# Kernel optimization log

Measured on AMD Instinct MI355X. Metric: run time of the kernel, lower is better.

The kernel has to match this reference:

```python
import jax, jax.numpy as jnp
import numpy as np

N_WIRES = 10
N_BLOCKS = 4
DIM = 2 ** N_WIRES


def _tables(n):
    # Basis-state bit tables. Wire 0 is the most-significant bit (torchquantum convention).
    s = np.arange(2 ** n)
    bits = (s[None, :] >> (n - 1 - np.arange(n))[:, None]) & 1  # [n, 2^n]
    zval = (1 - 2 * bits).astype(np.float32)  # PauliZ eigenvalue per wire per basis state
    # Composition of the circular CNOT ring (0,1),(1,2),...,(n-2,n-1),(n-1,0)
    # as a single basis permutation: state'[s] = state[P[s]].
    pairs = [(i, i + 1) for i in range(n - 1)] + [(n - 1, 0)]
    P = s.copy()
    for c, t in pairs:
        bit = (s >> (n - 1 - c)) & 1
        g = s ^ (bit << (n - 1 - t))  # CNOT maps new[s] = old[g(s)]
        P = P[g]
    return zval, P


_ZVAL_NP, _PERM_NP = _tables(N_WIRES)


def setup_inputs() -> dict:
    key = jax.random.key(0)
    k1, k2 = jax.random.split(key)
    x = jax.random.normal(k1, (2048, N_WIRES), jnp.float32)
    params = jax.random.normal(k2, (N_BLOCKS, 6, N_WIRES), jnp.float32)
    return {"x": x, "params": params}


def _rz_all(state, theta, zval):
    # RZ(theta_w) on every wire fused into one diagonal phase over the full statevector.
    # RZ = diag(e^{-i t/2}, e^{+i t/2}); exponent sign = -zval (bit0 -> -1).
    phase = jnp.exp((-0.5j) * (theta @ zval).astype(jnp.complex64))  # [2^n]
    return state * phase[None, :]


def _ry_all(state, theta, bsz):
    # RY(theta_w) on each wire w: 2x2 rotation applied along that wire's axis.
    for w in range(N_WIRES):
        left = 2 ** w
        right = DIM // (2 * left)
        s4 = state.reshape(bsz, left, 2, right)
        c = jnp.cos(theta[w] * 0.5)
        s_ = jnp.sin(theta[w] * 0.5)
        U = jnp.stack([jnp.stack([c, -s_]), jnp.stack([s_, c])]).astype(jnp.complex64)
        s4 = jnp.einsum('bixk,jx->bijk', s4, U)
        state = s4.reshape(bsz, DIM)
    return state


def reference(x, params):
    zval = jnp.asarray(_ZVAL_NP)
    perm = jnp.asarray(_PERM_NP)
    bsz = x.shape[0]
    state = jnp.zeros((bsz, DIM), jnp.complex64).at[:, 0].set(1.0)  # |0...0>
    for k in range(N_BLOCKS):
        p = params[k]
        # NOTE: the original module's "rx" layers are constructed with tq.RZ,
        # so each block is RZ, RY, RZ, CNOT-ring, RZ, RY, RZ, CNOT-ring.
        state = _rz_all(state, p[0], zval)
        state = _ry_all(state, p[1], bsz)
        state = _rz_all(state, p[2], zval)
        state = state[:, perm]
        state = _rz_all(state, p[3], zval)
        state = _ry_all(state, p[4], bsz)
        state = _rz_all(state, p[5], zval)
        state = state[:, perm]
        if k != N_BLOCKS - 1:
            # data re-uploading encoder: RZ(x[:, w]) on wire w, batch-dependent diagonal
            enc = jnp.exp((-0.5j) * (x @ zval).astype(jnp.complex64))  # [B, 2^n]
            state = state * enc
    probs = state.real ** 2 + state.imag ** 2  # [B, 2^n]
    out = probs @ zval.T  # MeasureAll PauliZ -> [B, n_wires]
    return out[None]  # [1, B, n_wires]
```

## Files before the change

### kernel.cpp

```cpp
#include <hip/hip_runtime.h>

#define NW 10

typedef float v2f __attribute__((ext_vector_type(2)));
typedef float v4f __attribute__((ext_vector_type(4)));

template<int CTRL>
__device__ __forceinline__ float fdpp(float v) {
    return __int_as_float(__builtin_amdgcn_mov_dpp(__float_as_int(v), CTRL, 0xF, 0xF, true));
}
template<int PAT>
__device__ __forceinline__ float fswz(float v) {
    return __int_as_float(__builtin_amdgcn_ds_swizzle(__float_as_int(v), PAT));
}

__device__ __forceinline__ int sC(int W, int lane, int r) { return (W << 8) | (lane << 2) | r; }
__device__ __forceinline__ int sL1(int W, int lane, int r) {
    return ((r & 1) << 8) | (((r >> 1) & 1) << 9)
         | ((lane & 1) << 4) | (((lane >> 1) & 1) << 6) | (((lane >> 2) & 1) << 2)
         | (((lane >> 3) & 1) << 7) | (((lane >> 4) & 1) << 3) | (((lane >> 5) & 1) << 5)
         | ((W & 1) << 0) | (((W >> 1) & 1) << 1);
}
__device__ __forceinline__ int phi(int e) {
    return e ^ ((e & 0x10) >> 1) ^ ((e & 0x20) >> 4);
}

__global__ void precompute_kernel(const float* __restrict__ params, float4* __restrict__ tab4) {
    const int d = blockIdx.x;
    const int j = threadIdx.x;
    if (d < 14) {
        int k, row; bool L1;
        if (d < 3)       { k = d + 1;  row = 0; L1 = false; }
        else if (d < 7)  { k = d - 3;  row = 2; L1 = true;  }
        else if (d < 11) { k = d - 7;  row = 3; L1 = false; }
        else             { k = d - 11; row = 5; L1 = true;  }
        const float* th = params + (k * 6 + row) * NW;
        const int W = j >> 8, lane = j & 63, r = (j >> 6) & 3;
        const int s = L1 ? sL1(W, lane, r) : sC(W, lane, r);
        float ang = 0.f;
#pragma unroll
        for (int w = 0; w < NW; ++w)
            ang += th[w] * (((s >> (9 - w)) & 1) ? 0.5f : -0.5f);
        float sn, cs;
        __sincosf(ang, &sn, &cs);
        tab4[d * 1024 + j] = make_float4(cs, sn, -sn, cs);
    } else if (j < 80) {
        const int ry = j / NW, w = j % NW;
        const int k = ry >> 1, i = ry & 1;
        const float* th = params + (k * 6 + (i ? 4 : 1)) * NW;
        float sn, cs;
        __sincosf(0.5f * th[w], &sn, &cs);
        float2* ryt = (float2*)(tab4 + 14 * 1024);
        ryt[j] = make_float2(cs, sn);
    }
}

__global__ __launch_bounds__(256, 4) void qsim_kernel(const float* __restrict__ x,
                                                      const v4f* __restrict__ tab4,
                                                      float* __restrict__ out) {
    __shared__ v2f buf[2][1024];
    __shared__ float sred[4][NW];

    const int t     = threadIdx.x;
    const int W     = t >> 6;
    const int lane  = t & 63;
    const int b     = blockIdx.x;
    const int ebase = lane | (W << 8);
    const float2* ry_tab = (const float2*)(tab4 + 14 * 1024);

    v2f st[4];
#pragma unroll
    for (int r = 0; r < 4; ++r) st[r] = (v2f){0.f, 0.f};
    if (t == 0) st[0].x = 1.f;

    const int wbase = phi(ebase);
    const int l0 = lane & 1, l1 = (lane >> 1) & 1, l2 = (lane >> 2) & 1,
              l3 = (lane >> 3) & 1, l4 = (lane >> 4) & 1, l5 = (lane >> 5) & 1;
    const int W0 = W & 1, W1 = (W >> 1) & 1;
    const int riA0 = l2 | (l4 << 1) | (l0 << 2) | (l5 << 3) | (l1 << 4) | (l3 << 5) | (W << 6);
    const int rgA  = phi(riA0);
    const int g0 = (l2 ^ l3) | ((l4 ^ l5) << 1) | ((l0 ^ l1) << 2) | ((l5 ^ W0) << 3)
                 | ((l1 ^ l2) << 4) | ((l3 ^ l4) << 5)
                 | ((W0 ^ W1) << 6) | (W1 << 7) | (l0 << 9);
    const int gP = phi(g0);

    const float* xb = x + b * NW;
    v2f xp[4];
    {
        float xv[NW];
#pragma unroll
        for (int w = 0; w < NW; ++w) xv[w] = xb[w];
        float A = 0.f;
#pragma unroll
        for (int w = 0; w < NW; ++w) A += xv[w];
        float hi = -0.5f * A;
        if (W & 2) hi += xv[0];
        if (W & 1) hi += xv[1];
#pragma unroll
        for (int j = 0; j < 6; ++j)
            hi += ((lane >> j) & 1) ? xv[7 - j] : 0.f;
        float lo[4];
        lo[0] = 0.f;   lo[1] = xv[9];
        lo[2] = xv[8]; lo[3] = xv[8] + xv[9];
#pragma unroll
        for (int r = 0; r < 4; ++r) {
            float sn, cs;
            __sincosf(hi + lo[r], &sn, &cs);
            xp[r] = (v2f){cs, sn};
        }
    }

    int bs = 0;
    v4f tq[4];

    auto pre = [&](int d) {
        const v4f* tb = tab4 + (d << 10) + ebase;
#pragma unroll
        for (int r = 0; r < 4; ++r) tq[r] = tb[r << 6];
    };
    auto apply_t = [&]() {
#pragma unroll
        for (int r = 0; r < 4; ++r)
            st[r] = st[r].x * tq[r].xy + st[r].y * tq[r].zw;
    };
    auto apply_tx = [&]() {
#pragma unroll
        for (int r = 0; r < 4; ++r) {
            const v2f c = xp[r].x * tq[r].xy + xp[r].y * tq[r].zw;
            const v2f cq = (v2f){-c.y, c.x};
            st[r] = st[r].x * c + st[r].y * cq;
        }
    };

    auto bfly_local = [&](float2 cw, int m) {
#pragma unroll
        for (int r = 0; r < 4; ++r) {
            if (!(r & m)) {
                const int r2 = r | m;
                const v2f a = st[r];
                st[r]  = cw.x * a - cw.y * st[r2];
                st[r2] = cw.y * a + cw.x * st[r2];
            }
        }
    };

    auto ry = [&](int ridx) {
        const float2* rt = ry_tab + ridx * NW;
        bfly_local(rt[9], 1);
        bfly_local(rt[8], 2);
        {   const float2 cw = rt[7]; const float ss = (lane & 1) ? cw.y : -cw.y;
#pragma unroll
            for (int r = 0; r < 4; ++r) {
                v2f p; p.x = fdpp<0xB1>(st[r].x); p.y = fdpp<0xB1>(st[r].y);
                st[r] = cw.x * st[r] + ss * p;
            }
        }
        {   const float2 cw = rt[6]; const float ss = (lane & 2) ? cw.y : -cw.y;
#pragma unroll
            for (int r = 0; r < 4; ++r) {
                v2f p; p.x = fdpp<0x4E>(st[r].x); p.y = fdpp<0x4E>(st[r].y);
                st[r] = cw.x * st[r] + ss * p;
            }
        }
        {   const float2 cw = rt[4]; const float ss = (lane & 8) ? cw.y : -cw.y;
#pragma unroll
            for (int r = 0; r < 4; ++r) {
                v2f p; p.x = fdpp<0x128>(st[r].x); p.y = fdpp<0x128>(st[r].y);
                st[r] = cw.x * st[r] + ss * p;
            }
        }
        {
            v2f* B = buf[bs]; bs ^= 1;
#pragma unroll
            for (int r = 0; r < 4; ++r)
                B[wbase + (r << 6)] = st[r];
            __syncthreads();
#pragma unroll
            for (int r = 0; r < 4; ++r)
                st[r] = B[rgA + (r << 8)];
        }
        bfly_local(rt[1], 1);
        bfly_local(rt[0], 2);
        {   const float2 cw = rt[5]; const float ss = (lane & 1) ? cw.y : -cw.y;
#pragma unroll
            for (int r = 0; r < 4; ++r) {
                v2f p; p.x = fdpp<0xB1>(st[r].x); p.y = fdpp<0xB1>(st[r].y);
                st[r] = cw.x * st[r] + ss * p;
            }
        }
        {   const float2 cw = rt[3]; const float ss = (lane & 2) ? cw.y : -cw.y;
#pragma unroll
            for (int r = 0; r < 4; ++r) {
                v2f p; p.x = fdpp<0x4E>(st[r].x); p.y = fdpp<0x4E>(st[r].y);
                st[r] = cw.x * st[r] + ss * p;
            }
        }
        {   const float2 cw = rt[2]; const float ss = (lane & 8) ? cw.y : -cw.y;
#pragma unroll
            for (int r = 0; r < 4; ++r) {
                v2f p; p.x = fdpp<0x128>(st[r].x); p.y = fdpp<0x128>(st[r].y);
                st[r] = cw.x * st[r] + ss * p;
            }
        }
    };

    auto perm = [&]() {
        v2f* B = buf[bs]; bs ^= 1;
#pragma unroll
        for (int r = 0; r < 4; ++r)
            B[wbase + (r << 6)] = st[r];
        __syncthreads();
        constexpr int xc[4] = {0, 0x1C0, 0x300, 0x2C0};
#pragma unroll
        for (int r = 0; r < 4; ++r)
            st[r] = B[gP ^ xc[r]];
    };

#pragma unroll 1
    for (int k = 0; k < 4; ++k) {
        if (k > 0) apply_tx();
        pre(3 + k);
        ry(2 * k);
        apply_t();
        pre(7 + k);
        perm();
        apply_t();
        if (k < 3) pre(11 + k);
        ry(2 * k + 1);
        if (k < 3) { apply_t(); pre(k); }
        perm();
    }

    float pr[4];
#pragma unroll
    for (int r = 0; r < 4; ++r) pr[r] = st[r].x * st[r].x + st[r].y * st[r].y;
    float S = 0.f;
#pragma unroll
    for (int r = 0; r < 4; ++r) S += pr[r];

    float acc[NW];
    acc[0] = (W & 2) ? -S : S;
    acc[1] = (W & 1) ? -S : S;
#pragma unroll
    for (int w = 2; w <= 7; ++w) {
        const int j = 7 - w;
        acc[w] = ((lane >> j) & 1) ? -S : S;
    }
    {
        float t8 = 0.f, t9 = 0.f;
#pragma unroll
        for (int r = 0; r < 4; ++r) {
            t8 += (r & 2) ? -pr[r] : pr[r];
            t9 += (r & 1) ? -pr[r] : pr[r];
        }
        acc[8] = t8; acc[9] = t9;
    }
#pragma unroll
    for (int w = 0; w < NW; ++w) {
        float a = acc[w];
        a += fdpp<0xB1>(a);
        a += fdpp<0x4E>(a);
        a += fswz<0x101F>(a);
        a += fdpp<0x128>(a);
        a += fswz<0x401F>(a);
        a += __shfl_xor(a, 32, 64);
        acc[w] = a;
    }
    if (lane == 0) {
#pragma unroll
        for (int w = 0; w < NW; ++w) sred[W][w] = acc[w];
    }
    __syncthreads();
    if (t < NW) out[b * NW + t] = sred[0][t] + sred[1][t] + sred[2][t] + sred[3][t];
}

extern "C" void kernel_launch(void* const* d_in, const int* in_sizes, int n_in,
                              void* d_out, int out_size, void* d_ws, size_t ws_size,
                              hipStream_t stream) {
    const float* x      = (const float*)d_in[0];
    const float* params = (const float*)d_in[1];
    float* out          = (float*)d_out;
    float4* tab4        = (float4*)d_ws;
    (void)in_sizes; (void)n_in; (void)out_size; (void)ws_size;
    precompute_kernel<<<15, 1024, 0, stream>>>(params, tab4);
    qsim_kernel<<<2048, 256, 0, stream>>>(x, (const v4f*)tab4, out);
}
```

Baseline: 83.49 us.

## Change statevector register layout for vectorized LDS writes and skip final permutation

Thread t now owns four contiguous basis states instead of lane-strided ones. This lets each thread store its registers to LDS as two 16-byte writes with a new XOR swizzle, and lets phase tables load as contiguous float4s. The last CNOT-ring permutation and its barrier are dropped. The permutation is instead folded into the final PauliZ measurement through XOR parity signs. The new index mapping must be exactly consistent across the RY exchange, the permutation and the table generation, or results are wrong.

Measured after the change: 85.77 us. 2.7% more time.

```diff
diff --git a/kernel.cpp b/kernel.cpp
--- a/kernel.cpp
+++ b/kernel.cpp
@@ -14,16 +14,13 @@
     return __int_as_float(__builtin_amdgcn_ds_swizzle(__float_as_int(v), PAT));
 }
 
-__device__ __forceinline__ int sC(int W, int lane, int r) { return (W << 8) | (lane << 2) | r; }
 __device__ __forceinline__ int sL1(int W, int lane, int r) {
     return ((r & 1) << 8) | (((r >> 1) & 1) << 9)
          | ((lane & 1) << 4) | (((lane >> 1) & 1) << 6) | (((lane >> 2) & 1) << 2)
          | (((lane >> 3) & 1) << 7) | (((lane >> 4) & 1) << 3) | (((lane >> 5) & 1) << 5)
          | ((W & 1) << 0) | (((W >> 1) & 1) << 1);
 }
-__device__ __forceinline__ int phi(int e) {
-    return e ^ ((e & 0x10) >> 1) ^ ((e & 0x20) >> 4);
-}
+__device__ __forceinline__ int phiA(int a) { return a ^ ((a & 0x50) >> 3); }
 
 __global__ void precompute_kernel(const float* __restrict__ params, float4* __restrict__ tab4) {
     const int d = blockIdx.x;
@@ -35,8 +32,7 @@
         else if (d < 11) { k = d - 7;  row = 3; L1 = false; }
         else             { k = d - 11; row = 5; L1 = true;  }
         const float* th = params + (k * 6 + row) * NW;
-        const int W = j >> 8, lane = j & 63, r = (j >> 6) & 3;
-        const int s = L1 ? sL1(W, lane, r) : sC(W, lane, r);
+        const int s = L1 ? sL1(j >> 8, (j >> 2) & 63, j & 3) : j;
         float ang = 0.f;
 #pragma unroll
         for (int w = 0; w < NW; ++w)
@@ -58,14 +54,13 @@
 __global__ __launch_bounds__(256, 4) void qsim_kernel(const float* __restrict__ x,
                                                       const v4f* __restrict__ tab4,
                                                       float* __restrict__ out) {
-    __shared__ v2f buf[2][1024];
+    __shared__ __align__(16) v2f buf[2][1024];
     __shared__ float sred[4][NW];
 
     const int t     = threadIdx.x;
     const int W     = t >> 6;
     const int lane  = t & 63;
     const int b     = blockIdx.x;
-    const int ebase = lane | (W << 8);
     const float2* ry_tab = (const float2*)(tab4 + 14 * 1024);
 
     v2f st[4];
@@ -73,16 +68,16 @@
     for (int r = 0; r < 4; ++r) st[r] = (v2f){0.f, 0.f};
     if (t == 0) st[0].x = 1.f;
 
-    const int wbase = phi(ebase);
     const int l0 = lane & 1, l1 = (lane >> 1) & 1, l2 = (lane >> 2) & 1,
               l3 = (lane >> 3) & 1, l4 = (lane >> 4) & 1, l5 = (lane >> 5) & 1;
     const int W0 = W & 1, W1 = (W >> 1) & 1;
-    const int riA0 = l2 | (l4 << 1) | (l0 << 2) | (l5 << 3) | (l1 << 4) | (l3 << 5) | (W << 6);
-    const int rgA  = phi(riA0);
-    const int g0 = (l2 ^ l3) | ((l4 ^ l5) << 1) | ((l0 ^ l1) << 2) | ((l5 ^ W0) << 3)
-                 | ((l1 ^ l2) << 4) | ((l3 ^ l4) << 5)
-                 | ((W0 ^ W1) << 6) | (W1 << 7) | (l0 << 9);
-    const int gP = phi(g0);
+
+    const int wb4 = (t << 1) ^ (l4 << 2) ^ l2;
+    const int rgA2 = phiA(sL1(W, lane, 0));
+    const int abase = (W0 ^ W1) | (W1 << 1) | ((l2 ^ l3) << 2) | ((l4 ^ l5) << 3)
+                    | ((l0 ^ l1) << 4) | ((l5 ^ W0) << 5) | ((l1 ^ l2) << 6)
+                    | ((l3 ^ l4) << 7) | (l0 << 9);
+    const int gP2 = phiA(abase);
 
     const float* xb = x + b * NW;
     v2f xp[4];
@@ -114,9 +109,9 @@
     v4f tq[4];
 
     auto pre = [&](int d) {
-        const v4f* tb = tab4 + (d << 10) + ebase;
-#pragma unroll
-        for (int r = 0; r < 4; ++r) tq[r] = tb[r << 6];
+        const v4f* tb = tab4 + (d << 10) + (t << 2);
+#pragma unroll
+        for (int r = 0; r < 4; ++r) tq[r] = tb[r];
     };
     auto apply_t = [&]() {
 #pragma unroll
@@ -144,6 +139,12 @@
         }
     };
 
+    auto lds_write_own = [&](v2f* B) {
+        v4f* B4 = (v4f*)B;
+        B4[wb4]     = (v4f){st[0].x, st[0].y, st[1].x, st[1].y};
+        B4[wb4 ^ 1] = (v4f){st[2].x, st[2].y, st[3].x, st[3].y};
+    };
+
     auto ry = [&](int ridx) {
         const float2* rt = ry_tab + ridx * NW;
         bfly_local(rt[9], 1);
@@ -171,13 +172,11 @@
         }
         {
             v2f* B = buf[bs]; bs ^= 1;
+            lds_write_own(B);
+            __syncthreads();
 #pragma unroll
             for (int r = 0; r < 4; ++r)
-                B[wbase + (r << 6)] = st[r];
-            __syncthreads();
-#pragma unroll
-            for (int r = 0; r < 4; ++r)
-                st[r] = B[rgA + (r << 8)];
+                st[r] = B[rgA2 + (r << 8)];
         }
         bfly_local(rt[1], 1);
         bfly_local(rt[0], 2);
@@ -206,14 +205,12 @@
 
     auto perm = [&]() {
         v2f* B = buf[bs]; bs ^= 1;
+        lds_write_own(B);
+        __syncthreads();
+        constexpr int xq[4] = {0, 0x103, 0x300, 0x203};
 #pragma unroll
         for (int r = 0; r < 4; ++r)
-            B[wbase + (r << 6)] = st[r];
-        __syncthreads();
-        constexpr int xc[4] = {0, 0x1C0, 0x300, 0x2C0};
-#pragma unroll
-        for (int r = 0; r < 4; ++r)
-            st[r] = B[gP ^ xc[r]];
+            st[r] = B[gP2 ^ xq[r]];
     };
 
 #pragma unroll 1
@@ -227,34 +224,35 @@
         apply_t();
         if (k < 3) pre(11 + k);
         ry(2 * k + 1);
-        if (k < 3) { apply_t(); pre(k); }
-        perm();
+        if (k < 3) { apply_t(); pre(k); perm(); }
     }
 
     float pr[4];
 #pragma unroll
     for (int r = 0; r < 4; ++r) pr[r] = st[r].x * st[r].x + st[r].y * st[r].y;
-    float S = 0.f;
-#pragma unroll
-    for (int r = 0; r < 4; ++r) S += pr[r];
+    const float D = pr[0] - pr[1] - pr[2] + pr[3];
+    const float E = pr[0] - pr[1] + pr[2] - pr[3];
+    const int g2 = l3;
+    const int g3 = g2 ^ l1;
+    const int g4 = g3 ^ l5;
+    const int g5 = g4 ^ l0;
+    const int g6 = g5 ^ l4;
+    const int g7 = g6 ^ l2;
+    const int g8 = g7 ^ W1;
+    const int g9 = g8 ^ W0;
 
     float acc[NW];
-    acc[0] = (W & 2) ? -S : S;
-    acc[1] = (W & 1) ? -S : S;
-#pragma unroll
-    for (int w = 2; w <= 7; ++w) {
-        const int j = 7 - w;
-        acc[w] = ((lane >> j) & 1) ? -S : S;
-    }
-    {
-        float t8 = 0.f, t9 = 0.f;
-#pragma unroll
-        for (int r = 0; r < 4; ++r) {
-            t8 += (r & 2) ? -pr[r] : pr[r];
-            t9 += (r & 1) ? -pr[r] : pr[r];
-        }
-        acc[8] = t8; acc[9] = t9;
-    }
+    acc[0] = g9 ? -E : E;
+    acc[1] = D;
+    acc[2] = g2 ? -D : D;
+    acc[3] = g3 ? -D : D;
+    acc[4] = g4 ? -D : D;
+    acc[5] = g5 ? -D : D;
+    acc[6] = g6 ? -D : D;
+    acc[7] = g7 ? -D : D;
+    acc[8] = g8 ? -D : D;
+    acc[9] = g9 ? -D : D;
+
 #pragma unroll
     for (int w = 0; w < NW; ++w) {
         float a = acc[w];
```

## Merge RZ phase tables across CNOT-ring permutation to halve diagonal applications

Applied to the files above, without the earlier changes.

Combines pairs of RZ diagonals separated by the CNOT-ring permutation into a single precomputed phase table by mapping basis indices through the permutation (q = s ^ s>>1 ...). The main loop now applies one diagonal per half-block instead of two, and the precompute kernel builds 7 tables instead of 14. This cuts complex multiplies and table loads per layer, but relies on the new index mapping matching the in-register layout; a mistake there would silently give wrong results.

Result: faster. 80.13 us (-4.0%).

```diff
diff --git a/kernel.cpp b/kernel.cpp
--- a/kernel.cpp
+++ b/kernel.cpp
@@ -14,13 +14,6 @@
     return __int_as_float(__builtin_amdgcn_ds_swizzle(__float_as_int(v), PAT));
 }
 
-__device__ __forceinline__ int sC(int W, int lane, int r) { return (W << 8) | (lane << 2) | r; }
-__device__ __forceinline__ int sL1(int W, int lane, int r) {
-    return ((r & 1) << 8) | (((r >> 1) & 1) << 9)
-         | ((lane & 1) << 4) | (((lane >> 1) & 1) << 6) | (((lane >> 2) & 1) << 2)
-         | (((lane >> 3) & 1) << 7) | (((lane >> 4) & 1) << 3) | (((lane >> 5) & 1) << 5)
-         | ((W & 1) << 0) | (((W >> 1) & 1) << 1);
-}
 __device__ __forceinline__ int phi(int e) {
     return e ^ ((e & 0x10) >> 1) ^ ((e & 0x20) >> 4);
 }
@@ -28,19 +21,26 @@
 __global__ void precompute_kernel(const float* __restrict__ params, float4* __restrict__ tab4) {
     const int d = blockIdx.x;
     const int j = threadIdx.x;
-    if (d < 14) {
-        int k, row; bool L1;
-        if (d < 3)       { k = d + 1;  row = 0; L1 = false; }
-        else if (d < 7)  { k = d - 3;  row = 2; L1 = true;  }
-        else if (d < 11) { k = d - 7;  row = 3; L1 = false; }
-        else             { k = d - 11; row = 5; L1 = true;  }
-        const float* th = params + (k * 6 + row) * NW;
+    if (d < 7) {
         const int W = j >> 8, lane = j & 63, r = (j >> 6) & 3;
-        const int s = L1 ? sL1(W, lane, r) : sC(W, lane, r);
+        const int s = (W << 8) | (lane << 2) | r;
+        const int q = s ^ (s >> 1) ^ ((s & 1) * 0x300);
+        const float* thA;
+        const float* thB;
+        if (d < 4) {
+            thA = params + (d * 6 + 3) * NW;
+            thB = params + (d * 6 + 2) * NW;
+        } else {
+            const int k = d - 4;
+            thA = params + ((k + 1) * 6 + 0) * NW;
+            thB = params + (k * 6 + 5) * NW;
+        }
         float ang = 0.f;
 #pragma unroll
-        for (int w = 0; w < NW; ++w)
-            ang += th[w] * (((s >> (9 - w)) & 1) ? 0.5f : -0.5f);
+        for (int w = 0; w < NW; ++w) {
+            ang += thA[w] * (((s >> (9 - w)) & 1) ? 0.5f : -0.5f);
+            ang += thB[w] * (((q >> (9 - w)) & 1) ? 0.5f : -0.5f);
+        }
         float sn, cs;
         __sincosf(ang, &sn, &cs);
         tab4[d * 1024 + j] = make_float4(cs, sn, -sn, cs);
@@ -50,7 +50,7 @@
         const float* th = params + (k * 6 + (i ? 4 : 1)) * NW;
         float sn, cs;
         __sincosf(0.5f * th[w], &sn, &cs);
-        float2* ryt = (float2*)(tab4 + 14 * 1024);
+        float2* ryt = (float2*)(tab4 + 7 * 1024);
         ryt[j] = make_float2(cs, sn);
     }
 }
@@ -66,7 +66,7 @@
     const int lane  = t & 63;
     const int b     = blockIdx.x;
     const int ebase = lane | (W << 8);
-    const float2* ry_tab = (const float2*)(tab4 + 14 * 1024);
+    const float2* ry_tab = (const float2*)(tab4 + 7 * 1024);
 
     v2f st[4];
 #pragma unroll
@@ -218,17 +218,14 @@
 
 #pragma unroll 1
     for (int k = 0; k < 4; ++k) {
-        if (k > 0) apply_tx();
-        pre(3 + k);
+        pre(k);
         ry(2 * k);
-        apply_t();
-        pre(7 + k);
         perm();
         apply_t();
-        if (k < 3) pre(11 + k);
+        if (k < 3) pre(4 + k);
         ry(2 * k + 1);
-        if (k < 3) { apply_t(); pre(k); }
         perm();
+        if (k < 3) apply_tx();
     }
 
     float pr[4];
@@ -282,6 +279,6 @@
     float* out          = (float*)d_out;
     float4* tab4        = (float4*)d_ws;
     (void)in_sizes; (void)n_in; (void)out_size; (void)ws_size;
-    precompute_kernel<<<15, 1024, 0, stream>>>(params, tab4);
+    precompute_kernel<<<8, 1024, 0, stream>>>(params, tab4);
     qsim_kernel<<<2048, 256, 0, stream>>>(x, (const v4f*)tab4, out);
 }
```
